# Optimization experiments

Measured on AMD Instinct MI355X. Metric: run time of the kernel, lower is better.

Reference implementation:

```python
import jax, jax.numpy as jnp
import numpy as np

B, L, D_T, DH, ALPHA, DTE, H, NL, DFF = 256, 64, 768, 128, 48, 64, 8, 3, 512


def setup_inputs() -> dict:
    key = jax.random.key(0)
    ks = jax.random.split(key, 24)
    n = lambda i, shape, s=1.0: jax.random.normal(ks[i], shape, dtype=jnp.float32) * s
    return {
        "cls_emb": n(0, (B, L, D_T)),
        "note_times": jnp.sort(jax.random.uniform(ks[1], (B, L), dtype=jnp.float32) * 48.0, axis=-1),
        "note_counts": jax.random.randint(ks[2], (B,), 1, L + 1).astype(jnp.int32),
        "proj_w": n(3, (D_T, DH), D_T ** -0.5), "proj_b": jnp.zeros((DH,), jnp.float32),
        "te_w": n(4, (DTE,)), "te_b": n(5, (DTE,)),
        "wq": n(6, (DTE, DTE), DTE ** -0.5), "wk": n(7, (DTE, DTE), DTE ** -0.5),
        "tf_wq": n(8, (NL, DH, DH), DH ** -0.5), "tf_wk": n(9, (NL, DH, DH), DH ** -0.5),
        "tf_wv": n(10, (NL, DH, DH), DH ** -0.5), "tf_wo": n(11, (NL, DH, DH), DH ** -0.5),
        "tf_ln1_g": jnp.ones((NL, DH), jnp.float32), "tf_ln1_b": jnp.zeros((NL, DH), jnp.float32),
        "tf_w1": n(12, (NL, DH, DFF), DH ** -0.5), "tf_b1": jnp.zeros((NL, DFF), jnp.float32),
        "tf_w2": n(13, (NL, DFF, DH), DFF ** -0.5), "tf_b2": jnp.zeros((NL, DH), jnp.float32),
        "tf_ln2_g": jnp.ones((NL, DH), jnp.float32), "tf_ln2_b": jnp.zeros((NL, DH), jnp.float32),
        "cls_w1": n(14, (DH, DH // 2), DH ** -0.5), "cls_b1": jnp.zeros((DH // 2,), jnp.float32),
        "cls_w2": n(15, (DH // 2, 1), (DH // 2) ** -0.5), "cls_b2": jnp.zeros((1,), jnp.float32),
    }


def _ln(x, g, b):
    mu = x.mean(-1, keepdims=True)
    var = x.var(-1, keepdims=True)
    return (x - mu) * jax.lax.rsqrt(var + 1e-5) * g + b


def _time_embed(t, w, b):
    # mTAND time embedding: dim 0 linear, rest periodic (sin)
    lin = t[..., None] * w + b
    return jnp.concatenate([lin[..., :1], jnp.sin(lin[..., 1:])], axis=-1)


def _forward(cls_emb, note_times, note_counts, proj_w, proj_b, te_w, te_b, wq, wk,
             tf_wq, tf_wk, tf_wv, tf_wo, tf_ln1_g, tf_ln1_b, tf_w1, tf_b1,
             tf_w2, tf_b2, tf_ln2_g, tf_ln2_b, cls_w1, cls_b1, cls_w2, cls_b2):
    # project frozen Longformer CLS embeddings -> note embeddings [B, L, DH]
    note_emb = cls_emb @ proj_w + proj_b
    alpha_pts = jnp.arange(ALPHA, dtype=jnp.float32)
    q_te = _time_embed(alpha_pts, te_w, te_b)          # [A, DTE]
    k_te = _time_embed(note_times, te_w, te_b)         # [B, L, DTE]
    dk = DTE // H
    q = (q_te @ wq).reshape(ALPHA, H, dk)
    k = (k_te @ wk).reshape(B, L, H, dk)
    scores = jnp.einsum('ahd,blhd->bhal', q, k) / np.float32(np.sqrt(dk))
    valid = jnp.arange(L)[None, :] < note_counts[:, None]      # [B, L] ragged mask
    scores = jnp.where(valid[:, None, None, :], scores, jnp.float32(-1e9))
    attn = jax.nn.softmax(scores, axis=-1)                     # [B, H, A, L]
    # one batched interpolation replaces the per-patient / per-dim python loops
    x = jnp.einsum('bhal,blf->bahf', attn, note_emb).mean(axis=2)  # [B, A, DH]
    x = jnp.where((note_counts > 0)[:, None, None], x, 0.0)
    # 3-layer post-norm transformer encoder over the alpha time grid
    hd = DH // H
    for i in range(NL):
        qh = (x @ tf_wq[i]).reshape(B, ALPHA, H, hd)
        kh = (x @ tf_wk[i]).reshape(B, ALPHA, H, hd)
        vh = (x @ tf_wv[i]).reshape(B, ALPHA, H, hd)
        s = jnp.einsum('bqhd,bkhd->bhqk', qh, kh) / np.float32(np.sqrt(hd))
        a = jax.nn.softmax(s, axis=-1)
        o = jnp.einsum('bhqk,bkhd->bqhd', a, vh).reshape(B, ALPHA, DH) @ tf_wo[i]
        x = _ln(x + o, tf_ln1_g[i], tf_ln1_b[i])
        f = jax.nn.relu(x @ tf_w1[i] + tf_b1[i]) @ tf_w2[i] + tf_b2[i]
        x = _ln(x + f, tf_ln2_g[i], tf_ln2_b[i])
    last = x[:, -1, :]
    logits = jax.nn.relu(last @ cls_w1 + cls_b1) @ cls_w2 + cls_b2
    return logits


def reference(cls_emb, note_times, note_counts, proj_w, proj_b, te_w, te_b, wq, wk,
              tf_wq, tf_wk, tf_wv, tf_wo, tf_ln1_g, tf_ln1_b, tf_w1, tf_b1,
              tf_w2, tf_b2, tf_ln2_g, tf_ln2_b, cls_w1, cls_b1, cls_w2, cls_b2):
    return _forward(cls_emb, note_times, note_counts, proj_w, proj_b, te_w, te_b, wq, wk,
                    tf_wq, tf_wk, tf_wv, tf_wo, tf_ln1_g, tf_ln1_b, tf_w1, tf_b1,
                    tf_w2, tf_b2, tf_ln2_g, tf_ln2_b, cls_w1, cls_b1, cls_w2, cls_b2)
```

## Files before the change

kernel.cpp:

```cpp
#include <hip/hip_runtime.h>
#include <hip/hip_bf16.h>

#define B_   256
#define L_   64
#define DT_  768
#define DH_  128
#define AL_  48
#define DTE_ 64
#define H_   8
#define NL_  3
#define DFF_ 512

typedef __attribute__((ext_vector_type(4))) float f32x4;
typedef __attribute__((ext_vector_type(4))) unsigned int u32x4;
typedef __attribute__((ext_vector_type(2))) unsigned int u32x2;
typedef __attribute__((ext_vector_type(8))) short short8;

__device__ inline unsigned short f2bf(float f) {
    union { float f; unsigned u; } v; v.f = f;
    unsigned r = (v.u + 0x7FFFu + ((v.u >> 16) & 1u)) >> 16;
    return (unsigned short)r;
}
__device__ inline unsigned f2bf2(float a, float b) {
    return (unsigned)f2bf(a) | ((unsigned)f2bf(b) << 16);
}
__device__ inline float bf2f(unsigned short u) {
    union { unsigned u; float f; } v; v.u = ((unsigned)u) << 16; return v.f;
}
__device__ inline short8 ldg8(const unsigned short* p) {
    union { short8 s; u32x4 v; } r;
    r.v = *(const u32x4*)p;
    return r.s;
}
__device__ inline unsigned pk_f16(float a, float b) {
    unsigned r;
    asm("v_cvt_pkrtz_f16_f32 %0, %1, %2" : "=v"(r) : "v"(a), "v"(b));
    return r;
}
__device__ inline unsigned pk_max(unsigned a, unsigned b) {
    unsigned r;
    asm("v_pk_max_f16 %0, %1, %2" : "=v"(r) : "v"(a), "v"(b));
    return r;
}
__device__ inline float f16_lo(unsigned h) {
    float f; asm("v_cvt_f32_f16 %0, %1" : "=v"(f) : "v"(h)); return f;
}
__device__ inline float f16_hi(unsigned h) {
    float f; unsigned t = h >> 16;
    asm("v_cvt_f32_f16 %0, %1" : "=v"(f) : "v"(t)); return f;
}

struct TEnt { const float* src; int dstOff; int K; int N; int tile0; };
struct TTab { TEnt e[19]; };

__global__ __launch_bounds__(256) void prep_weights_kernel(
    TTab tab, int ntile, unsigned short* __restrict__ wt,
    const float* __restrict__ te_w, const float* __restrict__ te_b,
    const float* __restrict__ wq, float* __restrict__ q_allG)
{
    __shared__ unsigned short lds[64][72];
    __shared__ float qte[AL_ * 68];
    int tid = threadIdx.x;
    if ((int)blockIdx.x >= ntile) {
        for (int i = tid; i < AL_ * 64; i += 256) {
            int a = i >> 6, j = i & 63;
            float lin = fmaf((float)a, te_w[j], te_b[j]);
            qte[a * 68 + j] = (j == 0) ? lin : __sinf(lin);
        }
        __syncthreads();
        for (int i = tid; i < AL_ * 64; i += 256) {
            int a = i >> 6, d = i & 63;
            float s0 = 0.f, s1 = 0.f, s2 = 0.f, s3 = 0.f;
            for (int j = 0; j < 64; j += 4) {
                s0 = fmaf(qte[a * 68 + j],     wq[j * 64 + d],       s0);
                s1 = fmaf(qte[a * 68 + j + 1], wq[(j + 1) * 64 + d], s1);
                s2 = fmaf(qte[a * 68 + j + 2], wq[(j + 2) * 64 + d], s2);
                s3 = fmaf(qte[a * 68 + j + 3], wq[(j + 3) * 64 + d], s3);
            }
            q_allG[i] = (s0 + s1) + (s2 + s3);
        }
        return;
    }
    int ei = 0;
    #pragma unroll
    for (int j = 1; j < 19; ++j) if ((int)blockIdx.x >= tab.e[j].tile0) ei = j;
    TEnt e = tab.e[ei];
    int t = blockIdx.x - e.tile0;
    int tilesK = e.K >> 6;
    int tk = t % tilesK, tn = t / tilesK;
    #pragma unroll
    for (int p = 0; p < 16; ++p) {
        int kk = p * 4 + (tid >> 6);
        int n = tid & 63;
        float v = e.src[(size_t)(tk * 64 + kk) * e.N + tn * 64 + n];
        lds[n][kk] = f2bf(v);
    }
    __syncthreads();
    #pragma unroll
    for (int p = 0; p < 2; ++p) {
        int c = p * 256 + tid;
        int n = c >> 3, q = c & 7;
        u32x4 v = *(const u32x4*)(&lds[n][q * 8]);
        *(u32x4*)(&wt[(size_t)e.dstOff + (size_t)(tn * 64 + n) * e.K + tk * 64 + q * 8]) = v;
    }
}

__global__ __launch_bounds__(256) void gemm_proj_kernel(
    const float* __restrict__ A, const unsigned short* __restrict__ Wt,
    const float* __restrict__ bias, unsigned short* __restrict__ C,
    int M, int N, int K)
{
    __shared__ unsigned short As[32 * 64];
    __shared__ unsigned short Bs[128 * 64];
    int tid = threadIdx.x;
    int bm = blockIdx.x * 32;
    int wave = tid >> 6, lane = tid & 63;
    int wm = wave >> 1, wn = wave & 1;
    int g = lane >> 4, r16 = lane & 15;

    f32x4 acc[4] = {};

    for (int k0 = 0; k0 < K; k0 += 64) {
        #pragma unroll
        for (int p = 0; p < 2; ++p) {
            int row = p * 16 + (tid >> 4);
            int c4 = tid & 15;
            f32x4 v = *(const f32x4*)(&A[(size_t)(bm + row) * K + k0 + c4 * 4]);
            u32x2 w;
            w[0] = f2bf2(v[0], v[1]);
            w[1] = f2bf2(v[2], v[3]);
            *(u32x2*)(&As[row * 64 + ((c4 * 4) ^ ((row & 7) << 3))]) = w;
        }
        #pragma unroll
        for (int p = 0; p < 4; ++p) {
            int c = p * 256 + tid;
            int n = c >> 3, q = c & 7;
            u32x4 v = *(const u32x4*)(&Wt[(size_t)n * K + k0 + q * 8]);
            *(u32x4*)(&Bs[n * 64 + ((q * 8) ^ ((n & 7) << 3))]) = v;
        }
        __syncthreads();
        #pragma unroll
        for (int kk = 0; kk < 2; ++kk) {
            short8 af, bf[4];
            int co = kk * 32 + g * 8;
            {
                int row = wm * 16 + r16;
                af = *(const short8*)(&As[row * 64 + (co ^ ((row & 7) << 3))]);
            }
            #pragma unroll
            for (int ni = 0; ni < 4; ++ni) {
                int row = wn * 64 + ni * 16 + r16;
                bf[ni] = *(const short8*)(&Bs[row * 64 + (co ^ ((row & 7) << 3))]);
            }
            #pragma unroll
            for (int ni = 0; ni < 4; ++ni)
                acc[ni] = __builtin_amdgcn_mfma_f32_16x16x32_bf16(af, bf[ni], acc[ni], 0, 0, 0);
        }
        __syncthreads();
    }
    #pragma unroll
    for (int ni = 0; ni < 4; ++ni) {
        int col = wn * 64 + ni * 16 + r16;
        float bv = bias[col];
        #pragma unroll
        for (int r = 0; r < 4; ++r) {
            int row = bm + wm * 16 + g * 4 + r;
            C[(size_t)row * N + col] = f2bf(acc[ni][r] + bv);
        }
    }
}

__global__ __launch_bounds__(256) void first_attn_kernel(
    const float* __restrict__ note_times, const int* __restrict__ note_counts,
    const float* __restrict__ te_w, const float* __restrict__ te_b,
    const float* __restrict__ wk, const float* __restrict__ q_all,
    const unsigned short* __restrict__ note_emb,
    float* __restrict__ x_out, unsigned short* __restrict__ xbf_out)
{
    __shared__ union RU {
        float kkL[64 * 68];
        unsigned short E[32 * 256];
        struct { unsigned short As[32 * 64]; unsigned short Bs[128 * 64]; } mm;
    } ru;
    __shared__ float rsL[32][8];

    const int bx = blockIdx.x;
    const int b = bx >> 1, a0 = (bx & 1) * 24;
    const int tid = threadIdx.x, lane = tid & 63;
    const int wv = __builtin_amdgcn_readfirstlane(tid >> 6);
    const int g = lane >> 4, r16 = lane & 15;
    const int nc = note_counts[b];

    float kte[64];
    {
        float t = note_times[b * 64 + lane];
        #pragma unroll
        for (int j = 0; j < 64; ++j) {
            float lin = fmaf(t, te_w[j], te_b[j]);
            kte[j] = (j == 0) ? lin : __sinf(lin);
        }
    }
    {
        float kvp[16] = {};
        #pragma unroll
        for (int j = 0; j < 64; ++j) {
            #pragma unroll
            for (int dd = 0; dd < 16; ++dd)
                kvp[dd] = fmaf(kte[j], wk[j * 64 + wv * 16 + dd], kvp[dd]);
        }
        #pragma unroll
        for (int q4 = 0; q4 < 4; ++q4)
            *(f32x4*)(&ru.kkL[lane * 68 + wv * 16 + q4 * 4]) = *(const f32x4*)(&kvp[q4 * 4]);
    }
    __syncthreads();
    float kv[64];
    #pragma unroll
    for (int q4 = 0; q4 < 16; ++q4)
        *(f32x4*)(&kv[q4 * 4]) = *(const f32x4*)(&ru.kkL[lane * 68 + q4 * 4]);
    __syncthreads();

    float abar[6] = {};
    const float scale = 0.35355339059327373f;
    #pragma unroll
    for (int p = 0; p < 2; ++p) {
        float e_reg[6][4];
        #pragma unroll
        for (int i = 0; i < 6; ++i) {
            int a = wv * 6 + i;
            float s[4];
            #pragma unroll
            for (int h = 0; h < 4; ++h) {
                float acc = 0.f;
                #pragma unroll
                for (int d = 0; d < 8; ++d)
                    acc = fmaf(q_all[(a0 + a) * 64 + p * 32 + h * 8 + d],
                               kv[p * 32 + h * 8 + d], acc);
                s[h] = (lane < nc) ? acc * scale : -1e9f;
            }
            unsigned m0 = pk_f16(s[0], s[1]);
            unsigned m1 = pk_f16(s[2], s[3]);
            #pragma unroll
            for (int st = 32; st >= 1; st >>= 1) {
                m0 = pk_max(m0, (unsigned)__shfl_xor((int)m0, st));
                m1 = pk_max(m1, (unsigned)__shfl_xor((int)m1, st));
            }
            float mm[4] = { f16_lo(m0), f16_hi(m0), f16_lo(m1), f16_hi(m1) };
            #pragma unroll
            for (int h = 0; h < 4; ++h) {
                float e = __expf(s[h] - mm[h]);
                e_reg[i][h] = e;
                int k = h * 64 + lane;
                ru.E[a * 256 + (k ^ ((a & 7) << 3))] = f2bf(e);
            }
        }
        __syncthreads();
        if (wv < 2) {
            f32x4 acc = {0.f, 0.f, 0.f, 0.f};
            #pragma unroll
            for (int ks = 0; ks < 8; ++ks) {
                int row = wv * 16 + r16;
                short8 af = *(const short8*)(&ru.E[row * 256 + ((ks * 32 + g * 8) ^ ((row & 7) << 3))]);
                short bb = (r16 == (ks >> 1)) ? (short)0x3F80 : (short)0;
                short8 bf = { bb, bb, bb, bb, bb, bb, bb, bb };
                acc = __builtin_amdgcn_mfma_f32_16x16x32_bf16(af, bf, acc, 0, 0, 0);
            }
            if (r16 < 4) {
                #pragma unroll
                for (int r = 0; r < 4; ++r)
                    rsL[wv * 16 + g * 4 + r][p * 4 + r16] = 0.125f / fmaxf(acc[r], 1e-20f);
            }
        }
        __syncthreads();
        #pragma unroll
        for (int i = 0; i < 6; ++i) {
            int a = wv * 6 + i;
            f32x4 rv = *(const f32x4*)(&rsL[a][p * 4]);
            abar[i] = fmaf(e_reg[i][0], rv[0], abar[i]);
            abar[i] = fmaf(e_reg[i][1], rv[1], abar[i]);
            abar[i] = fmaf(e_reg[i][2], rv[2], abar[i]);
            abar[i] = fmaf(e_reg[i][3], rv[3], abar[i]);
        }
    }
    {
        int l = tid & 63;
        #pragma unroll
        for (int pp = 0; pp < 4; ++pp) {
            int c = pp * 4 + (tid >> 6);
            u32x4 v = *(const u32x4*)(&note_emb[((size_t)b * 64 + l) * 128 + c * 8]);
            #pragma unroll
            for (int j = 0; j < 8; ++j) {
                unsigned short h16 = (unsigned short)((j & 1) ? (v[j >> 1] >> 16) : (v[j >> 1] & 0xffff));
                int f = c * 8 + j;
                ru.mm.Bs[f * 64 + (l ^ ((f & 7) << 3))] = h16;
            }
        }
    }
    #pragma unroll
    for (int i = 0; i < 6; ++i) {
        int a = wv * 6 + i;
        ru.mm.As[a * 64 + (lane ^ ((a & 7) << 3))] = f2bf(abar[i]);
    }
    __syncthreads();

    f32x4 pv[4] = {};
    #pragma unroll
    for (int q = 0; q < 4; ++q) {
        int f = wv * 4 + q, mi = f >> 3, ni = f & 7;
        #pragma unroll
        for (int ks = 0; ks < 2; ++ks) {
            int co = ks * 32 + g * 8;
            int raw = mi * 16 + r16, rb = ni * 16 + r16;
            short8 af = *(const short8*)(&ru.mm.As[raw * 64 + (co ^ ((raw & 7) << 3))]);
            short8 bf = *(const short8*)(&ru.mm.Bs[rb * 64 + (co ^ ((rb & 7) << 3))]);
            pv[q] = __builtin_amdgcn_mfma_f32_16x16x32_bf16(af, bf, pv[q], 0, 0, 0);
        }
    }
    #pragma unroll
    for (int q = 0; q < 4; ++q) {
        int f = wv * 4 + q, mi = f >> 3, ni = f & 7;
        #pragma unroll
        for (int r = 0; r < 4; ++r) {
            int row = mi * 16 + g * 4 + r;
            if (row < 24) {
                float v = (nc > 0) ? pv[q][r] : 0.f;
                size_t o = ((size_t)b * AL_ + a0 + row) * 128 + ni * 16 + r16;
                x_out[o] = v;
                xbf_out[o] = f2bf(v);
            }
        }
    }
}

__global__ __launch_bounds__(192) void attn2_kernel(
    const unsigned short* __restrict__ xbf, const unsigned short* __restrict__ WtL,
    unsigned short* __restrict__ o)
{
    __shared__ union UA {
        unsigned short Xs[AL_ * 128];
        float sL[AL_ * 52];
    } ua;
    __shared__ union UB {
        struct { unsigned short qM[AL_ * 40]; unsigned short kM[AL_ * 40]; } qk;
        unsigned short P[AL_ * 64];
    } ub;
    __shared__ unsigned short vT[16 * 72];
    int bid = blockIdx.x;
    int b = bid >> 3, h = bid & 7;
    int tid = threadIdx.x, lane = tid & 63;
    int wv = __builtin_amdgcn_readfirstlane(tid >> 6);
    int g = lane >> 4, r16 = lane & 15;

    #pragma unroll
    for (int p = 0; p < 4; ++p) {
        int i = p * 192 + tid;
        int a = i >> 4, c = (i & 15) * 8;
        u32x4 v = *(const u32x4*)(&xbf[((size_t)b * AL_ + a) * 128 + c]);
        *(u32x4*)(&ua.Xs[a * 128 + (c & 64) + ((c & 63) ^ ((a & 7) << 3))]) = v;
    }
    for (int i = tid; i < 768; i += 192) {
        int a = i >> 4, k2 = 16 + (i & 15);
        ub.qk.qM[a * 40 + k2] = 0;
        ub.qk.kM[a * 40 + k2] = 0;
    }
    for (int i = tid; i < 256; i += 192) {
        int d = i >> 4, k2 = 48 + (i & 15);
        vT[d * 72 + k2] = 0;
    }
    __syncthreads();

    {
        f32x4 acc[3] = {};
        const unsigned short* Wm = WtL + wv * 16384 + (size_t)(h * 16) * 128;
        #pragma unroll
        for (int kq = 0; kq < 4; ++kq) {
            short8 bf = ldg8(&Wm[(size_t)r16 * 128 + kq * 32 + g * 8]);
            #pragma unroll
            for (int mi = 0; mi < 3; ++mi) {
                int row = mi * 16 + r16;
                int c = kq * 32 + g * 8;
                short8 af = *(const short8*)(&ua.Xs[row * 128 + (c & 64) + ((c & 63) ^ ((row & 7) << 3))]);
                acc[mi] = __builtin_amdgcn_mfma_f32_16x16x32_bf16(af, bf, acc[mi], 0, 0, 0);
            }
        }
        #pragma unroll
        for (int mi = 0; mi < 3; ++mi) {
            #pragma unroll
            for (int r = 0; r < 4; ++r) {
                int a = mi * 16 + g * 4 + r;
                unsigned short hv = f2bf(acc[mi][r]);
                if (wv == 0) ub.qk.qM[a * 40 + r16] = hv;
                else if (wv == 1) ub.qk.kM[a * 40 + r16] = hv;
                else vT[r16 * 72 + a] = hv;
            }
        }
    }
    __syncthreads();

    {
        #pragma unroll
        for (int ni = 0; ni < 3; ++ni) {
            f32x4 acc = {0.f, 0.f, 0.f, 0.f};
            short8 af = *(const short8*)(&ub.qk.qM[(wv * 16 + r16) * 40 + g * 8]);
            short8 bf = *(const short8*)(&ub.qk.kM[(ni * 16 + r16) * 40 + g * 8]);
            acc = __builtin_amdgcn_mfma_f32_16x16x32_bf16(af, bf, acc, 0, 0, 0);
            #pragma unroll
            for (int r = 0; r < 4; ++r)
                ua.sL[(wv * 16 + g * 4 + r) * 52 + ni * 16 + r16] = acc[r] * 0.25f;
        }
    }
    __syncthreads();

    {
        int row = wv * 16 + (lane >> 2), sub = lane & 3;
        f32x4 v0 = *(const f32x4*)(&ua.sL[row * 52 + sub * 4]);
        f32x4 v1 = *(const f32x4*)(&ua.sL[row * 52 + 16 + sub * 4]);
        f32x4 v2 = *(const f32x4*)(&ua.sL[row * 52 + 32 + sub * 4]);
        float m = fmaxf(fmaxf(fmaxf(v0[0], v0[1]), fmaxf(v0[2], v0[3])),
                        fmaxf(fmaxf(v1[0], v1[1]), fmaxf(v1[2], v1[3])));
        m = fmaxf(m, fmaxf(fmaxf(v2[0], v2[1]), fmaxf(v2[2], v2[3])));
        m = fmaxf(m, __shfl_xor(m, 1));
        m = fmaxf(m, __shfl_xor(m, 2));
        float e[12];
        #pragma unroll
        for (int j = 0; j < 4; ++j) {
            e[j]     = __expf(v0[j] - m);
            e[4 + j] = __expf(v1[j] - m);
            e[8 + j] = __expf(v2[j] - m);
        }
        float sum = 0.f;
        #pragma unroll
        for (int j = 0; j < 12; ++j) sum += e[j];
        sum += __shfl_xor(sum, 1);
        sum += __shfl_xor(sum, 2);
        float inv = __fdividef(1.f, sum);
        #pragma unroll
        for (int c = 0; c < 3; ++c) {
            u32x2 w;
            w[0] = f2bf2(e[c * 4 + 0] * inv, e[c * 4 + 1] * inv);
            w[1] = f2bf2(e[c * 4 + 2] * inv, e[c * 4 + 3] * inv);
            int col = c * 16 + sub * 4;
            *(u32x2*)(&ub.P[row * 64 + (col ^ ((row & 7) << 3))]) = w;
        }
        for (int i = tid; i < 768; i += 192) {
            int a = i >> 4, c = 48 + (i & 15);
            ub.P[a * 64 + (c ^ ((a & 7) << 3))] = 0;
        }
    }
    __syncthreads();

    {
        f32x4 acc = {0.f, 0.f, 0.f, 0.f};
        #pragma unroll
        for (int ks = 0; ks < 2; ++ks) {
            int co = ks * 32 + g * 8;
            int rp = wv * 16 + r16;
            short8 af = *(const short8*)(&ub.P[rp * 64 + (co ^ ((rp & 7) << 3))]);
            short8 bf = *(const short8*)(&vT[r16 * 72 + co]);
            acc = __builtin_amdgcn_mfma_f32_16x16x32_bf16(af, bf, acc, 0, 0, 0);
        }
        #pragma unroll
        for (int r = 0; r < 4; ++r) {
            int a = wv * 16 + g * 4 + r;
            o[((size_t)b * AL_ + a) * 128 + h * 16 + r16] = f2bf(acc[r]);
        }
    }
}

template<int ROWS>
__global__ __launch_bounds__(256) void layer_tail_kernel(
    const unsigned short* __restrict__ obuf, const unsigned short* __restrict__ Wl,
    const float* __restrict__ b1, const float* __restrict__ b2,
    const float* __restrict__ g1, const float* __restrict__ be1,
    const float* __restrict__ g2, const float* __restrict__ be2,
    float* __restrict__ x, unsigned short* __restrict__ xbf,
    int last, const float* __restrict__ cw1, const float* __restrict__ cb1,
    const float* __restrict__ cw2, const float* __restrict__ cb2,
    float* __restrict__ outp)
{
    constexpr int MR = ROWS / 16;
    __shared__ unsigned short OX[ROWS * 128];
    __shared__ union { unsigned short hid[ROWS * 512]; float Cs[ROWS * 132]; } u2;
    __shared__ float xr[ROWS * 132];
    const int tid = threadIdx.x, lane = tid & 63;
    const int wv = __builtin_amdgcn_readfirstlane(tid >> 6);
    const int g = lane >> 4, r16 = lane & 15;
    const int row0 = last ? ((int)blockIdx.x * 48 + 32) : ((int)blockIdx.x * ROWS);

    #pragma unroll
    for (int p = 0; p < MR; ++p) {
        int i = p * 256 + tid;
        int a = i >> 4, c = (i & 15) * 8;
        u32x4 v = *(const u32x4*)(&obuf[(size_t)(row0 + a) * 128 + c]);
        *(u32x4*)(&OX[a * 128 + (c & 64) + ((c & 63) ^ ((a & 7) << 3))]) = v;
    }
    __syncthreads();

    {
        f32x4 wacc[MR][2] = {};
        #pragma unroll
        for (int q = 0; q < 2; ++q) {
            int ni = wv * 2 + q;
            const unsigned short* Wm = Wl + 49152 + (size_t)(ni * 16 + r16) * 128;
            #pragma unroll
            for (int kq = 0; kq < 4; ++kq) {
                int co = kq * 32 + g * 8;
                short8 bf = ldg8(Wm + co);
                #pragma unroll
                for (int mi = 0; mi < MR; ++mi) {
                    int ra = mi * 16 + r16;
                    short8 af = *(const short8*)(&OX[ra * 128 + (co & 64) + ((co & 63) ^ ((ra & 7) << 3))]);
                    wacc[mi][q] = __builtin_amdgcn_mfma_f32_16x16x32_bf16(af, bf, wacc[mi][q], 0, 0, 0);
                }
            }
        }
        #pragma unroll
        for (int mi = 0; mi < MR; ++mi)
            #pragma unroll
            for (int q = 0; q < 2; ++q) {
                int ni = wv * 2 + q;
                #pragma unroll
                for (int r = 0; r < 4; ++r)
                    u2.Cs[(mi * 16 + g * 4 + r) * 132 + ni * 16 + r16] = wacc[mi][q][r];
            }
    }
    __syncthreads();

    #pragma unroll
    for (int rr = 0; rr < ROWS / 4; ++rr) {
        int row = wv * (ROWS / 4) + rr;
        size_t go = (size_t)(row0 + row) * 128;
        float v0 = u2.Cs[row * 132 + lane] + x[go + lane];
        float v1 = u2.Cs[row * 132 + 64 + lane] + x[go + 64 + lane];
        float sum = v0 + v1, sq = v0 * v0 + v1 * v1;
        #pragma unroll
        for (int o2 = 32; o2 >= 1; o2 >>= 1) {
            sum += __shfl_xor(sum, o2);
            sq  += __shfl_xor(sq, o2);
        }
        float mu = sum * (1.f / 128.f);
        float var = sq * (1.f / 128.f) - mu * mu;
        float rs = rsqrtf(var + 1e-5f);
        float o0 = (v0 - mu) * rs * g1[lane] + be1[lane];
        float o1 = (v1 - mu) * rs * g1[lane + 64] + be1[lane + 64];
        xr[row * 132 + lane] = o0;
        xr[row * 132 + 64 + lane] = o1;
        OX[row * 128 + (lane ^ ((row & 7) << 3))] = f2bf(o0);
        OX[row * 128 + 64 + (lane ^ ((row & 7) << 3))] = f2bf(o1);
    }
    __syncthreads();

    {
        f32x4 hacc[MR][8] = {};
        #pragma unroll
        for (int nf = 0; nf < 8; ++nf) {
            int col = wv * 128 + nf * 16 + r16;
            const unsigned short* Wm = Wl + 65536 + (size_t)col * 128;
            #pragma unroll
            for (int kq = 0; kq < 4; ++kq) {
                int co = kq * 32 + g * 8;
                short8 bf = ldg8(Wm + co);
                #pragma unroll
                for (int mi = 0; mi < MR; ++mi) {
                    int ra = mi * 16 + r16;
                    short8 af = *(const short8*)(&OX[ra * 128 + (co & 64) + ((co & 63) ^ ((ra & 7) << 3))]);
                    hacc[mi][nf] = __builtin_amdgcn_mfma_f32_16x16x32_bf16(af, bf, hacc[mi][nf], 0, 0, 0);
                }
            }
        }
        #pragma unroll
        for (int nf = 0; nf < 8; ++nf) {
            int col = wv * 128 + nf * 16 + r16;
            float bv = b1[col];
            #pragma unroll
            for (int mi = 0; mi < MR; ++mi)
                #pragma unroll
                for (int r = 0; r < 4; ++r) {
                    int rowa = mi * 16 + g * 4 + r;
                    u2.hid[rowa * 512 + (col & 448) + ((col & 63) ^ ((rowa & 7) << 3))] =
                        f2bf(fmaxf(hacc[mi][nf][r] + bv, 0.f));
                }
        }
    }
    __syncthreads();

    f32x4 yacc[MR][2] = {};
    #pragma unroll
    for (int q = 0; q < 2; ++q) {
        int ni = wv * 2 + q;
        const unsigned short* Wm = Wl + 131072 + (size_t)(ni * 16 + r16) * 512;
        #pragma unroll
        for (int kq = 0; kq < 16; ++kq) {
            int co = kq * 32 + g * 8;
            short8 bf = ldg8(Wm + co);
            #pragma unroll
            for (int mi = 0; mi < MR; ++mi) {
                int ra = mi * 16 + r16;
                short8 af = *(const short8*)(&u2.hid[ra * 512 + (co & 448) + ((co & 63) ^ ((ra & 7) << 3))]);
                yacc[mi][q] = __builtin_amdgcn_mfma_f32_16x16x32_bf16(af, bf, yacc[mi][q], 0, 0, 0);
            }
        }
    }
    __syncthreads();
    #pragma unroll
    for (int mi = 0; mi < MR; ++mi)
        #pragma unroll
        for (int q = 0; q < 2; ++q) {
            int ni = wv * 2 + q;
            float bv = b2[ni * 16 + r16];
            #pragma unroll
            for (int r = 0; r < 4; ++r)
                u2.Cs[(mi * 16 + g * 4 + r) * 132 + ni * 16 + r16] = yacc[mi][q][r] + bv;
        }
    __syncthreads();

    #pragma unroll
    for (int rr = 0; rr < ROWS / 4; ++rr) {
        int row = wv * (ROWS / 4) + rr;
        size_t go = (size_t)(row0 + row) * 128;
        float v0 = u2.Cs[row * 132 + lane] + xr[row * 132 + lane];
        float v1 = u2.Cs[row * 132 + 64 + lane] + xr[row * 132 + 64 + lane];
        float sum = v0 + v1, sq = v0 * v0 + v1 * v1;
        #pragma unroll
        for (int o2 = 32; o2 >= 1; o2 >>= 1) {
            sum += __shfl_xor(sum, o2);
            sq  += __shfl_xor(sq, o2);
        }
        float mu = sum * (1.f / 128.f);
        float var = sq * (1.f / 128.f) - mu * mu;
        float rs = rsqrtf(var + 1e-5f);
        float o0 = (v0 - mu) * rs * g2[lane] + be2[lane];
        float o1 = (v1 - mu) * rs * g2[lane + 64] + be2[lane + 64];
        if (!last) {
            x[go + lane] = o0;
            x[go + 64 + lane] = o1;
            xbf[go + lane] = f2bf(o0);
            xbf[go + 64 + lane] = f2bf(o1);
        } else {
            xr[row * 132 + lane] = o0;
            xr[row * 132 + 64 + lane] = o1;
        }
    }
    if (last) {
        __syncthreads();
        if (wv == 0) {
            float hj = cb1[lane];
            #pragma unroll 8
            for (int d = 0; d < 128; ++d)
                hj = fmaf(xr[(ROWS - 1) * 132 + d], cw1[d * 64 + lane], hj);
            hj = fmaxf(hj, 0.f);
            float acc = hj * cw2[lane];
            #pragma unroll
            for (int o2 = 32; o2 >= 1; o2 >>= 1) acc += __shfl_xor(acc, o2);
            if (lane == 0) outp[blockIdx.x] = acc + cb2[0];
        }
    }
}

extern "C" void kernel_launch(void* const* d_in, const int* in_sizes, int n_in,
                              void* d_out, int out_size, void* d_ws, size_t ws_size,
                              hipStream_t stream) {
    (void)in_sizes; (void)n_in; (void)out_size; (void)ws_size;
    const float* cls_emb    = (const float*)d_in[0];
    const float* note_times = (const float*)d_in[1];
    const int*   note_counts= (const int*)d_in[2];
    const float* proj_w     = (const float*)d_in[3];
    const float* proj_b     = (const float*)d_in[4];
    const float* te_w       = (const float*)d_in[5];
    const float* te_b       = (const float*)d_in[6];
    const float* wq         = (const float*)d_in[7];
    const float* wk         = (const float*)d_in[8];
    const float* tf_wq      = (const float*)d_in[9];
    const float* tf_wk      = (const float*)d_in[10];
    const float* tf_wv      = (const float*)d_in[11];
    const float* tf_wo      = (const float*)d_in[12];
    const float* tf_ln1_g   = (const float*)d_in[13];
    const float* tf_ln1_b   = (const float*)d_in[14];
    const float* tf_w1      = (const float*)d_in[15];
    const float* tf_b1      = (const float*)d_in[16];
    const float* tf_w2      = (const float*)d_in[17];
    const float* tf_b2      = (const float*)d_in[18];
    const float* tf_ln2_g   = (const float*)d_in[19];
    const float* tf_ln2_b   = (const float*)d_in[20];
    const float* cls_w1     = (const float*)d_in[21];
    const float* cls_b1     = (const float*)d_in[22];
    const float* cls_w2     = (const float*)d_in[23];
    const float* cls_b2     = (const float*)d_in[24];
    float* out = (float*)d_out;
    float* ws = (float*)d_ws;

    unsigned short* note_emb16 = (unsigned short*)(ws + 0);
    float* x        = ws + 1048576;
    unsigned short* obuf16 = (unsigned short*)(ws + 2621440);
    unsigned short* xbf    = (unsigned short*)(ws + 3407872);
    float* q_all    = ws + 4194304;
    unsigned short* wt     = (unsigned short*)(ws + 4197376);

    TTab tab;
    int tile = 0, idx = 0;
    auto add = [&](const float* src, int dstOff, int K, int N) {
        tab.e[idx].src = src; tab.e[idx].dstOff = dstOff;
        tab.e[idx].K = K; tab.e[idx].N = N; tab.e[idx].tile0 = tile;
        tile += (K / 64) * (N / 64); ++idx;
    };
    add(proj_w, 0, DT_, DH_);
    int layerBase[NL_];
    for (int i = 0; i < NL_; ++i) {
        int base = 98304 + i * 196608;
        layerBase[i] = base;
        add(tf_wq + (size_t)i * DH_ * DH_, base,           DH_, DH_);
        add(tf_wk + (size_t)i * DH_ * DH_, base + 16384,   DH_, DH_);
        add(tf_wv + (size_t)i * DH_ * DH_, base + 32768,   DH_, DH_);
        add(tf_wo + (size_t)i * DH_ * DH_, base + 49152,   DH_, DH_);
        add(tf_w1 + (size_t)i * DH_ * DFF_, base + 65536,  DH_, DFF_);
        add(tf_w2 + (size_t)i * DFF_ * DH_, base + 131072, DFF_, DH_);
    }
    prep_weights_kernel<<<tile + 1, 256, 0, stream>>>(tab, tile, wt, te_w, te_b, wq, q_all);

    const int Mx = B_ * AL_;

    gemm_proj_kernel<<<(B_ * L_) / 32, 256, 0, stream>>>(
        cls_emb, wt, proj_b, note_emb16, B_ * L_, DH_, DT_);

    first_attn_kernel<<<B_ * 2, 256, 0, stream>>>(
        note_times, note_counts, te_w, te_b, wk, q_all, note_emb16, x, xbf);

    for (int i = 0; i < NL_; ++i) {
        int base = layerBase[i];
        int last = (i == NL_ - 1);
        attn2_kernel<<<B_ * H_, 192, 0, stream>>>(xbf, wt + base, obuf16);
        if (!last) {
            layer_tail_kernel<32><<<Mx / 32, 256, 0, stream>>>(
                obuf16, wt + base,
                tf_b1 + i * DFF_, tf_b2 + i * DH_,
                tf_ln1_g + i * DH_, tf_ln1_b + i * DH_,
                tf_ln2_g + i * DH_, tf_ln2_b + i * DH_,
                x, xbf,
                0, cls_w1, cls_b1, cls_w2, cls_b2, out);
        } else {
            layer_tail_kernel<16><<<B_, 256, 0, stream>>>(
                obuf16, wt + base,
                tf_b1 + i * DFF_, tf_b2 + i * DH_,
                tf_ln1_g + i * DH_, tf_ln1_b + i * DH_,
                tf_ln2_g + i * DH_, tf_ln2_b + i * DH_,
                x, xbf,
                1, cls_w1, cls_b1, cls_w2, cls_b2, out);
        }
    }
}
```

Before: 174.0 us.

## Process two heads per attention block and stream projection weights directly

The projection GEMM drops its LDS staging of the weight tile. It uses a 128-wide K step and reads the B fragments straight from global memory, with each wave covering two N tiles across both M tiles. The per-layer attention kernel now handles two heads per block, so each block loads the X tile into LDS once for both heads, and the grid shrinks by half. This cuts redundant X loads and LDS traffic, but the two heads run serially inside a block with extra barriers, and there are fewer blocks to spread across the GPU.

```diff
diff --git a/kernel.cpp b/kernel.cpp
--- a/kernel.cpp
+++ b/kernel.cpp
@@ -110,62 +110,62 @@
     const float* __restrict__ bias, unsigned short* __restrict__ C,
     int M, int N, int K)
 {
-    __shared__ unsigned short As[32 * 64];
-    __shared__ unsigned short Bs[128 * 64];
+    __shared__ unsigned short As[32 * 128];
     int tid = threadIdx.x;
     int bm = blockIdx.x * 32;
     int wave = tid >> 6, lane = tid & 63;
-    int wm = wave >> 1, wn = wave & 1;
     int g = lane >> 4, r16 = lane & 15;
 
-    f32x4 acc[4] = {};
-
-    for (int k0 = 0; k0 < K; k0 += 64) {
-        #pragma unroll
-        for (int p = 0; p < 2; ++p) {
-            int row = p * 16 + (tid >> 4);
-            int c4 = tid & 15;
-            f32x4 v = *(const f32x4*)(&A[(size_t)(bm + row) * K + k0 + c4 * 4]);
-            u32x2 w;
-            w[0] = f2bf2(v[0], v[1]);
-            w[1] = f2bf2(v[2], v[3]);
-            *(u32x2*)(&As[row * 64 + ((c4 * 4) ^ ((row & 7) << 3))]) = w;
-        }
-        #pragma unroll
-        for (int p = 0; p < 4; ++p) {
-            int c = p * 256 + tid;
-            int n = c >> 3, q = c & 7;
-            u32x4 v = *(const u32x4*)(&Wt[(size_t)n * K + k0 + q * 8]);
-            *(u32x4*)(&Bs[n * 64 + ((q * 8) ^ ((n & 7) << 3))]) = v;
-        }
-        __syncthreads();
-        #pragma unroll
-        for (int kk = 0; kk < 2; ++kk) {
-            short8 af, bf[4];
+    f32x4 acc[2][2] = {};
+
+    for (int k0 = 0; k0 < K; k0 += 128) {
+        {
+            int row = tid >> 3, c16 = (tid & 7) * 16;
+            const float* Ap = &A[(size_t)(bm + row) * K + k0 + c16];
+            f32x4 v0 = *(const f32x4*)(Ap);
+            f32x4 v1 = *(const f32x4*)(Ap + 4);
+            f32x4 v2 = *(const f32x4*)(Ap + 8);
+            f32x4 v3 = *(const f32x4*)(Ap + 12);
+            u32x4 w0, w1;
+            w0[0] = f2bf2(v0[0], v0[1]); w0[1] = f2bf2(v0[2], v0[3]);
+            w0[2] = f2bf2(v1[0], v1[1]); w0[3] = f2bf2(v1[2], v1[3]);
+            w1[0] = f2bf2(v2[0], v2[1]); w1[1] = f2bf2(v2[2], v2[3]);
+            w1[2] = f2bf2(v3[0], v3[1]); w1[3] = f2bf2(v3[2], v3[3]);
+            int cA = c16, cB = c16 + 8;
+            *(u32x4*)(&As[row * 128 + (cA & 64) + ((cA & 63) ^ ((row & 7) << 3))]) = w0;
+            *(u32x4*)(&As[row * 128 + (cB & 64) + ((cB & 63) ^ ((row & 7) << 3))]) = w1;
+        }
+        __syncthreads();
+        #pragma unroll
+        for (int kk = 0; kk < 4; ++kk) {
             int co = kk * 32 + g * 8;
-            {
-                int row = wm * 16 + r16;
-                af = *(const short8*)(&As[row * 64 + (co ^ ((row & 7) << 3))]);
-            }
-            #pragma unroll
-            for (int ni = 0; ni < 4; ++ni) {
-                int row = wn * 64 + ni * 16 + r16;
-                bf[ni] = *(const short8*)(&Bs[row * 64 + (co ^ ((row & 7) << 3))]);
-            }
-            #pragma unroll
-            for (int ni = 0; ni < 4; ++ni)
-                acc[ni] = __builtin_amdgcn_mfma_f32_16x16x32_bf16(af, bf[ni], acc[ni], 0, 0, 0);
-        }
-        __syncthreads();
-    }
-    #pragma unroll
-    for (int ni = 0; ni < 4; ++ni) {
-        int col = wn * 64 + ni * 16 + r16;
+            short8 af[2];
+            #pragma unroll
+            for (int mi = 0; mi < 2; ++mi) {
+                int rr = mi * 16 + r16;
+                af[mi] = *(const short8*)(&As[rr * 128 + (co & 64) + ((co & 63) ^ ((rr & 7) << 3))]);
+            }
+            #pragma unroll
+            for (int q = 0; q < 2; ++q) {
+                int ni = wave * 2 + q;
+                short8 bf = ldg8(&Wt[(size_t)(ni * 16 + r16) * K + k0 + co]);
+                acc[0][q] = __builtin_amdgcn_mfma_f32_16x16x32_bf16(af[0], bf, acc[0][q], 0, 0, 0);
+                acc[1][q] = __builtin_amdgcn_mfma_f32_16x16x32_bf16(af[1], bf, acc[1][q], 0, 0, 0);
+            }
+        }
+        __syncthreads();
+    }
+    #pragma unroll
+    for (int q = 0; q < 2; ++q) {
+        int col = (wave * 2 + q) * 16 + r16;
         float bv = bias[col];
         #pragma unroll
-        for (int r = 0; r < 4; ++r) {
-            int row = bm + wm * 16 + g * 4 + r;
-            C[(size_t)row * N + col] = f2bf(acc[ni][r] + bv);
+        for (int mi = 0; mi < 2; ++mi) {
+            #pragma unroll
+            for (int r = 0; r < 4; ++r) {
+                int row = bm + mi * 16 + g * 4 + r;
+                C[(size_t)row * N + col] = f2bf(acc[mi][q][r] + bv);
+            }
         }
     }
 }
@@ -335,17 +335,15 @@
     const unsigned short* __restrict__ xbf, const unsigned short* __restrict__ WtL,
     unsigned short* __restrict__ o)
 {
-    __shared__ union UA {
-        unsigned short Xs[AL_ * 128];
-        float sL[AL_ * 52];
-    } ua;
+    __shared__ unsigned short Xs[AL_ * 128];
+    __shared__ float sL[AL_ * 52];
     __shared__ union UB {
         struct { unsigned short qM[AL_ * 40]; unsigned short kM[AL_ * 40]; } qk;
         unsigned short P[AL_ * 64];
     } ub;
     __shared__ unsigned short vT[16 * 72];
     int bid = blockIdx.x;
-    int b = bid >> 3, h = bid & 7;
+    int b = bid >> 2, h0 = (bid & 3) << 1;
     int tid = threadIdx.x, lane = tid & 63;
     int wv = __builtin_amdgcn_readfirstlane(tid >> 6);
     int g = lane >> 4, r16 = lane & 15;
@@ -355,12 +353,7 @@
         int i = p * 192 + tid;
         int a = i >> 4, c = (i & 15) * 8;
         u32x4 v = *(const u32x4*)(&xbf[((size_t)b * AL_ + a) * 128 + c]);
-        *(u32x4*)(&ua.Xs[a * 128 + (c & 64) + ((c & 63) ^ ((a & 7) << 3))]) = v;
-    }
-    for (int i = tid; i < 768; i += 192) {
-        int a = i >> 4, k2 = 16 + (i & 15);
-        ub.qk.qM[a * 40 + k2] = 0;
-        ub.qk.kM[a * 40 + k2] = 0;
+        *(u32x4*)(&Xs[a * 128 + (c & 64) + ((c & 63) ^ ((a & 7) << 3))]) = v;
     }
     for (int i = tid; i < 256; i += 192) {
         int d = i >> 4, k2 = 48 + (i & 15);
@@ -368,101 +361,110 @@
     }
     __syncthreads();
 
-    {
-        f32x4 acc[3] = {};
-        const unsigned short* Wm = WtL + wv * 16384 + (size_t)(h * 16) * 128;
-        #pragma unroll
-        for (int kq = 0; kq < 4; ++kq) {
-            short8 bf = ldg8(&Wm[(size_t)r16 * 128 + kq * 32 + g * 8]);
+    for (int hh = 0; hh < 2; ++hh) {
+        int h = h0 + hh;
+        for (int i = tid; i < 768; i += 192) {
+            int a = i >> 4, k2 = 16 + (i & 15);
+            ub.qk.qM[a * 40 + k2] = 0;
+            ub.qk.kM[a * 40 + k2] = 0;
+        }
+        {
+            f32x4 acc[3] = {};
+            const unsigned short* Wm = WtL + wv * 16384 + (size_t)(h * 16) * 128;
+            #pragma unroll
+            for (int kq = 0; kq < 4; ++kq) {
+                short8 bf = ldg8(&Wm[(size_t)r16 * 128 + kq * 32 + g * 8]);
+                #pragma unroll
+                for (int mi = 0; mi < 3; ++mi) {
+                    int row = mi * 16 + r16;
+                    int c = kq * 32 + g * 8;
+                    short8 af = *(const short8*)(&Xs[row * 128 + (c & 64) + ((c & 63) ^ ((row & 7) << 3))]);
+                    acc[mi] = __builtin_amdgcn_mfma_f32_16x16x32_bf16(af, bf, acc[mi], 0, 0, 0);
+                }
+            }
             #pragma unroll
             for (int mi = 0; mi < 3; ++mi) {
-                int row = mi * 16 + r16;
-                int c = kq * 32 + g * 8;
-                short8 af = *(const short8*)(&ua.Xs[row * 128 + (c & 64) + ((c & 63) ^ ((row & 7) << 3))]);
-                acc[mi] = __builtin_amdgcn_mfma_f32_16x16x32_bf16(af, bf, acc[mi], 0, 0, 0);
-            }
-        }
-        #pragma unroll
-        for (int mi = 0; mi < 3; ++mi) {
+                #pragma unroll
+                for (int r = 0; r < 4; ++r) {
+                    int a = mi * 16 + g * 4 + r;
+                    unsigned short hv = f2bf(acc[mi][r]);
+                    if (wv == 0) ub.qk.qM[a * 40 + r16] = hv;
+                    else if (wv == 1) ub.qk.kM[a * 40 + r16] = hv;
+                    else vT[r16 * 72 + a] = hv;
+                }
+            }
+        }
+        __syncthreads();
+
+        {
+            #pragma unroll
+            for (int ni = 0; ni < 3; ++ni) {
+                f32x4 acc = {0.f, 0.f, 0.f, 0.f};
+                short8 af = *(const short8*)(&ub.qk.qM[(wv * 16 + r16) * 40 + g * 8]);
+                short8 bf = *(const short8*)(&ub.qk.kM[(ni * 16 + r16) * 40 + g * 8]);
+                acc = __builtin_amdgcn_mfma_f32_16x16x32_bf16(af, bf, acc, 0, 0, 0);
+                #pragma unroll
+                for (int r = 0; r < 4; ++r)
+                    sL[(wv * 16 + g * 4 + r) * 52 + ni * 16 + r16] = acc[r] * 0.25f;
+            }
+        }
+        __syncthreads();
+
+        {
+            int row = wv * 16 + (lane >> 2), sub = lane & 3;
+            f32x4 v0 = *(const f32x4*)(&sL[row * 52 + sub * 4]);
+            f32x4 v1 = *(const f32x4*)(&sL[row * 52 + 16 + sub * 4]);
+            f32x4 v2 = *(const f32x4*)(&sL[row * 52 + 32 + sub * 4]);
+            float m = fmaxf(fmaxf(fmaxf(v0[0], v0[1]), fmaxf(v0[2], v0[3])),
+                            fmaxf(fmaxf(v1[0], v1[1]), fmaxf(v1[2], v1[3])));
+            m = fmaxf(m, fmaxf(fmaxf(v2[0], v2[1]), fmaxf(v2[2], v2[3])));
+            m = fmaxf(m, __shfl_xor(m, 1));
+            m = fmaxf(m, __shfl_xor(m, 2));
+            float e[12];
+            #pragma unroll
+            for (int j = 0; j < 4; ++j) {
+                e[j]     = __expf(v0[j] - m);
+                e[4 + j] = __expf(v1[j] - m);
+                e[8 + j] = __expf(v2[j] - m);
+            }
+            float sum = 0.f;
+            #pragma unroll
+            for (int j = 0; j < 12; ++j) sum += e[j];
+            sum += __shfl_xor(sum, 1);
+            sum += __shfl_xor(sum, 2);
+            float inv = __fdividef(1.f, sum);
+            #pragma unroll
+            for (int c = 0; c < 3; ++c) {
+                u32x2 w;
+                w[0] = f2bf2(e[c * 4 + 0] * inv, e[c * 4 + 1] * inv);
+                w[1] = f2bf2(e[c * 4 + 2] * inv, e[c * 4 + 3] * inv);
+                int col = c * 16 + sub * 4;
+                *(u32x2*)(&ub.P[row * 64 + (col ^ ((row & 7) << 3))]) = w;
+            }
+            for (int i = tid; i < 768; i += 192) {
+                int a = i >> 4, c = 48 + (i & 15);
+                ub.P[a * 64 + (c ^ ((a & 7) << 3))] = 0;
+            }
+        }
+        __syncthreads();
+
+        {
+            f32x4 acc = {0.f, 0.f, 0.f, 0.f};
+            #pragma unroll
+            for (int ks = 0; ks < 2; ++ks) {
+                int co = ks * 32 + g * 8;
+                int rp = wv * 16 + r16;
+                short8 af = *(const short8*)(&ub.P[rp * 64 + (co ^ ((rp & 7) << 3))]);
+                short8 bf = *(const short8*)(&vT[r16 * 72 + co]);
+                acc = __builtin_amdgcn_mfma_f32_16x16x32_bf16(af, bf, acc, 0, 0, 0);
+            }
             #pragma unroll
             for (int r = 0; r < 4; ++r) {
-                int a = mi * 16 + g * 4 + r;
-                unsigned short hv = f2bf(acc[mi][r]);
-                if (wv == 0) ub.qk.qM[a * 40 + r16] = hv;
-                else if (wv == 1) ub.qk.kM[a * 40 + r16] = hv;
-                else vT[r16 * 72 + a] = hv;
-            }
-        }
-    }
-    __syncthreads();
-
-    {
-        #pragma unroll
-        for (int ni = 0; ni < 3; ++ni) {
-            f32x4 acc = {0.f, 0.f, 0.f, 0.f};
-            short8 af = *(const short8*)(&ub.qk.qM[(wv * 16 + r16) * 40 + g * 8]);
-            short8 bf = *(const short8*)(&ub.qk.kM[(ni * 16 + r16) * 40 + g * 8]);
-            acc = __builtin_amdgcn_mfma_f32_16x16x32_bf16(af, bf, acc, 0, 0, 0);
-            #pragma unroll
-            for (int r = 0; r < 4; ++r)
-                ua.sL[(wv * 16 + g * 4 + r) * 52 + ni * 16 + r16] = acc[r] * 0.25f;
-        }
-    }
-    __syncthreads();
-
-    {
-        int row = wv * 16 + (lane >> 2), sub = lane & 3;
-        f32x4 v0 = *(const f32x4*)(&ua.sL[row * 52 + sub * 4]);
-        f32x4 v1 = *(const f32x4*)(&ua.sL[row * 52 + 16 + sub * 4]);
-        f32x4 v2 = *(const f32x4*)(&ua.sL[row * 52 + 32 + sub * 4]);
-        float m = fmaxf(fmaxf(fmaxf(v0[0], v0[1]), fmaxf(v0[2], v0[3])),
-                        fmaxf(fmaxf(v1[0], v1[1]), fmaxf(v1[2], v1[3])));
-        m = fmaxf(m, fmaxf(fmaxf(v2[0], v2[1]), fmaxf(v2[2], v2[3])));
-        m = fmaxf(m, __shfl_xor(m, 1));
-        m = fmaxf(m, __shfl_xor(m, 2));
-        float e[12];
-        #pragma unroll
-        for (int j = 0; j < 4; ++j) {
-            e[j]     = __expf(v0[j] - m);
-            e[4 + j] = __expf(v1[j] - m);
-            e[8 + j] = __expf(v2[j] - m);
-        }
-        float sum = 0.f;
-        #pragma unroll
-        for (int j = 0; j < 12; ++j) sum += e[j];
-        sum += __shfl_xor(sum, 1);
-        sum += __shfl_xor(sum, 2);
-        float inv = __fdividef(1.f, sum);
-        #pragma unroll
-        for (int c = 0; c < 3; ++c) {
-            u32x2 w;
-            w[0] = f2bf2(e[c * 4 + 0] * inv, e[c * 4 + 1] * inv);
-            w[1] = f2bf2(e[c * 4 + 2] * inv, e[c * 4 + 3] * inv);
-            int col = c * 16 + sub * 4;
-            *(u32x2*)(&ub.P[row * 64 + (col ^ ((row & 7) << 3))]) = w;
-        }
-        for (int i = tid; i < 768; i += 192) {
-            int a = i >> 4, c = 48 + (i & 15);
-            ub.P[a * 64 + (c ^ ((a & 7) << 3))] = 0;
-        }
-    }
-    __syncthreads();
-
-    {
-        f32x4 acc = {0.f, 0.f, 0.f, 0.f};
-        #pragma unroll
-        for (int ks = 0; ks < 2; ++ks) {
-            int co = ks * 32 + g * 8;
-            int rp = wv * 16 + r16;
-            short8 af = *(const short8*)(&ub.P[rp * 64 + (co ^ ((rp & 7) << 3))]);
-            short8 bf = *(const short8*)(&vT[r16 * 72 + co]);
-            acc = __builtin_amdgcn_mfma_f32_16x16x32_bf16(af, bf, acc, 0, 0, 0);
-        }
-        #pragma unroll
-        for (int r = 0; r < 4; ++r) {
-            int a = wv * 16 + g * 4 + r;
-            o[((size_t)b * AL_ + a) * 128 + h * 16 + r16] = f2bf(acc[r]);
-        }
+                int a = wv * 16 + g * 4 + r;
+                o[((size_t)b * AL_ + a) * 128 + h * 16 + r16] = f2bf(acc[r]);
+            }
+        }
+        __syncthreads();
     }
 }
 
@@ -727,7 +729,7 @@
     for (int i = 0; i < NL_; ++i) {
         int base = layerBase[i];
         int last = (i == NL_ - 1);
-        attn2_kernel<<<B_ * H_, 192, 0, stream>>>(xbf, wt + base, obuf16);
+        attn2_kernel<<<B_ * 4, 192, 0, stream>>>(xbf, wt + base, obuf16);
         if (!last) {
             layer_tail_kernel<32><<<Mx / 32, 256, 0, stream>>>(
                 obuf16, wt + base,
```

After: 169.2 us. 1.03x faster.
